# Kernel optimization log

Measured on AMD Instinct MI355X. Metric: run time of the kernel, lower is better.

Reference implementation:

```python
import jax, jax.numpy as jnp
import numpy as np

B_SZ, SEQ_LEN, STATE_DIM, D_IN, D_OUT, KX = 8, 2048, 1024, 512, 512, 10


def setup_inputs() -> dict:
    key = jax.random.key(0)
    ks = jax.random.split(key, 7)
    inputs = jax.random.normal(ks[0], (B_SZ, SEQ_LEN, D_IN), dtype=jnp.float32)
    h0 = jax.random.normal(ks[1], (STATE_DIM,), dtype=jnp.float32)
    # exponential_decay_init(lam=15): x = clamp(-1/lam * log(1-u), max=1); A = (1-x)*sign
    u = jax.random.uniform(ks[2], (STATE_DIM,), dtype=jnp.float32)
    x = jnp.minimum(-(1.0 / 15.0) * jnp.log1p(-u), 1.0)
    sign = jnp.sign(jax.random.normal(ks[3], (STATE_DIM,), dtype=jnp.float32))
    A = (1.0 - x) * sign
    Bm = jax.random.normal(ks[4], (D_IN, STATE_DIM), dtype=jnp.float32) / D_IN
    C = jax.random.normal(ks[5], (STATE_DIM, D_OUT), dtype=jnp.float32) / STATE_DIM
    M = jax.random.normal(ks[6], (D_OUT, D_IN, KX), dtype=jnp.float32) / D_OUT
    return {"inputs": inputs, "h0": h0, "A": A, "B": Bm, "C": C, "M": M}


def _ar_preds(M, x):
    # Equivalent to einsum('oik,bli->bklo') + per-k roll + triu mask + sum over k:
    # ar[b,l,:] = sum_{i=0}^{k-1, i<=l} M[:,:,i] @ x[b, l-i, :]
    b, l, d_in = x.shape
    kx = M.shape[2]
    ar = jnp.einsum('oi,bli->blo', M[:, :, 0], x)
    for i in range(1, kx):
        x_shift = jnp.pad(x, ((0, 0), (i, 0), (0, 0)))[:, :l]  # shift right, zero-fill
        ar = ar + jnp.einsum('oi,bli->blo', M[:, :, i], x_shift)
    return ar


def reference(inputs, h0, A, B, C, M):
    b, l, d_in = inputs.shape
    state_dim = A.shape[0]
    # Project inputs once: u_t @ B for all t -> [b, l, s]
    uB = jnp.einsum('bli,is->bls', inputs, B)

    def step(h, u_t):
        h = A * h + u_t  # diagonal recurrence
        return h, h

    h_init = jnp.broadcast_to(h0, (b, state_dim))
    _, hs = jax.lax.scan(step, h_init, jnp.swapaxes(uB, 0, 1))  # [l, b, s]
    hs = jnp.swapaxes(hs, 0, 1)  # [b, l, s]
    lds_out = hs @ C  # [b, l, d_out]
    return lds_out + _ar_preds(M, inputs)
```

## Files before the change

### kernel.cpp

```cpp
#include <hip/hip_runtime.h>

#define B_SZ   8
#define SEQ    2048
#define PSEQ   (SEQ+16)
#define SDIM   1024
#define DIN    512
#define DOUT   512
#define KX     10
#define RTOT   (B_SZ*SEQ)
#define LC     64
#define NC     (SEQ/LC)

typedef __attribute__((ext_vector_type(8))) short short8;
typedef __attribute__((ext_vector_type(4))) float f32x4;
typedef __attribute__((ext_vector_type(4))) unsigned short bfx4;

#define OFF_XP   0UL
#define OFF_UB   16908288UL
#define OFF_HS   50462720UL
#define OFF_BT   84017152UL
#define OFF_CT   85065728UL
#define OFF_MT   86114304UL

__device__ __forceinline__ short f2bf(float f) {
  unsigned u = __builtin_bit_cast(unsigned, f);
  u += 0x7fffu + ((u >> 16) & 1u);
  return (short)(u >> 16);
}
__device__ __forceinline__ float bf2f(unsigned short b) {
  return __builtin_bit_cast(float, (unsigned)b << 16);
}

#define GLOAD16(gp, lp) __builtin_amdgcn_global_load_lds( \
    (const __attribute__((address_space(1))) void*)(gp), \
    (__attribute__((address_space(3))) void*)(lp), 16, 0, 0)
#define WAITVM(n) asm volatile("s_waitcnt vmcnt(" #n ")" ::: "memory")
#define LGKM0()   do { asm volatile("s_waitcnt lgkmcnt(0)" ::: "memory"); \
                       __builtin_amdgcn_sched_barrier(0); } while (0)
#define SBAR() __builtin_amdgcn_s_barrier()

__global__ void k_conv_x(const float* __restrict__ in, short* __restrict__ out) {
  const int NG = RTOT * (DIN / 8);
  for (int g = blockIdx.x * 256 + threadIdx.x; g < NG; g += 2048 * 256) {
    int r = g >> 6, c8 = g & 63;
    int b = r >> 11, t = r & 2047;
    const float4* p = reinterpret_cast<const float4*>(in) + (size_t)g * 2;
    float4 f0 = p[0], f1 = p[1];
    short8 o;
    o[0]=f2bf(f0.x); o[1]=f2bf(f0.y); o[2]=f2bf(f0.z); o[3]=f2bf(f0.w);
    o[4]=f2bf(f1.x); o[5]=f2bf(f1.y); o[6]=f2bf(f1.z); o[7]=f2bf(f1.w);
    *reinterpret_cast<short8*>(out + ((size_t)(b * PSEQ + 16 + t) * DIN + c8 * 8)) = o;
  }
}

__global__ void k_zero_pad(short* __restrict__ Xp) {
  int idx = blockIdx.x * 256 + threadIdx.x;
  if (idx >= B_SZ * 16 * (DIN / 8)) return;
  int b = idx >> 10, rem = idx & 1023;
  int row16 = rem >> 6, c8 = rem & 63;
  const short8 z = {0,0,0,0,0,0,0,0};
  *reinterpret_cast<short8*>(Xp + ((size_t)(b * PSEQ + row16) * DIN + c8 * 8)) = z;
}

__global__ void k_transpose_bf16(const float* __restrict__ in, short* __restrict__ out,
                                 int rows, int cols) {
  __shared__ float t[32][33];
  int bx = blockIdx.x * 32, by = blockIdx.y * 32;
  int tx = threadIdx.x & 31, ty = threadIdx.x >> 5;
  #pragma unroll
  for (int j = 0; j < 32; j += 8)
    t[ty + j][tx] = in[(size_t)(by + ty + j) * cols + (bx + tx)];
  __syncthreads();
  #pragma unroll
  for (int j = 0; j < 32; j += 8)
    out[(size_t)(bx + ty + j) * rows + (by + tx)] = f2bf(t[tx][ty + j]);
}

__global__ void k_prep_M(const float* __restrict__ M, short* __restrict__ Mt) {
  int idx = blockIdx.x * 256 + threadIdx.x;
  if (idx >= DOUT * DIN) return;
  int o = idx / DIN, i = idx - o * DIN;
  const float* src = M + ((size_t)o * DIN + i) * KX;
  #pragma unroll
  for (int t = 0; t < KX; ++t)
    Mt[((size_t)t * DOUT + o) * DIN + i] = f2bf(src[t]);
}

__global__ void k_scan_E(const short* __restrict__ uB, const float* __restrict__ A,
                         float* __restrict__ E) {
  int blk = blockIdx.x, tid = threadIdx.x;
  int b = blk >> 5, c = blk & 31;
  int s0 = tid * 4;
  const short* base = uB + ((size_t)b * SEQ + (size_t)c * LC) * SDIM + s0;
  float a[4], h[4];
  #pragma unroll
  for (int j = 0; j < 4; ++j) { a[j] = A[s0 + j]; h[j] = 0.f; }
  for (int t = 0; t < LC; ++t) {
    bfx4 v = *reinterpret_cast<const bfx4*>(base + (size_t)t * SDIM);
    #pragma unroll
    for (int j = 0; j < 4; ++j) h[j] = fmaf(a[j], h[j], bf2f(v[j]));
  }
  float* ep = E + (size_t)blk * SDIM + s0;
  #pragma unroll
  for (int j = 0; j < 4; ++j) ep[j] = h[j];
}

__global__ void k_scan_S(const float* __restrict__ E, const float* __restrict__ A,
                         const float* __restrict__ h0, float* __restrict__ Sb) {
  int blk = blockIdx.x, tid = threadIdx.x;
  int b = blk >> 2;
  int s = ((blk & 3) << 8) + tid;
  float a = A[s], ap = a;
  #pragma unroll
  for (int q = 0; q < 6; ++q) ap *= ap;
  float S = h0[s];
  for (int c = 0; c < NC; ++c) {
    size_t idx = ((size_t)b * NC + c) * SDIM + s;
    Sb[idx] = S;
    S = fmaf(ap, S, E[idx]);
  }
}

__global__ void k_scan_h(const short* __restrict__ uB, const float* __restrict__ A,
                         const float* __restrict__ Sb, short* __restrict__ hs) {
  int blk = blockIdx.x, tid = threadIdx.x;
  int b = blk >> 5, c = blk & 31;
  int s0 = tid * 4;
  const short* base = uB + ((size_t)b * SEQ + (size_t)c * LC) * SDIM + s0;
  short* hbase = hs + ((size_t)b * SEQ + (size_t)c * LC) * SDIM + s0;
  float a[4], h[4];
  #pragma unroll
  for (int j = 0; j < 4; ++j) {
    a[j] = A[s0 + j];
    h[j] = Sb[(size_t)blk * SDIM + s0 + j];
  }
  for (int t = 0; t < LC; ++t) {
    bfx4 v = *reinterpret_cast<const bfx4*>(base + (size_t)t * SDIM);
    bfx4 o;
    #pragma unroll
    for (int j = 0; j < 4; ++j) {
      h[j] = fmaf(a[j], h[j], bf2f(v[j]));
      o[j] = (unsigned short)f2bf(h[j]);
    }
    *reinterpret_cast<bfx4*>(hbase + (size_t)t * SDIM) = o;
  }
}

__device__ __forceinline__ void stage128(const short* __restrict__ g, int ld,
                                         short* l, int tid) {
  int rsub = tid >> 3;
  int slot = (tid & 7) ^ (rsub & 7);
  #pragma unroll
  for (int i = 0; i < 4; ++i) {
    int row = i * 32 + rsub;
    GLOAD16(g + (size_t)row * ld + slot * 8, l + row * 64 + (tid & 7) * 8);
  }
}

__device__ __forceinline__ void mfma_tile(const short* lA, int aoff, const short* lB,
                                          int lane, int wm, int wn, f32x4 acc[4][4]) {
  int lr = lane & 15;
  int h  = lane >> 4;
  #pragma unroll
  for (int kk = 0; kk < 2; ++kk) {
    int kslot = kk * 4 + h;
    short8 af[4], bfr[4];
    #pragma unroll
    for (int mi = 0; mi < 4; ++mi) {
      int row = aoff + wm * 64 + mi * 16 + lr;
      af[mi] = *reinterpret_cast<const short8*>(lA + row * 64 + ((kslot ^ (row & 7)) << 3));
    }
    #pragma unroll
    for (int ni = 0; ni < 4; ++ni) {
      int row = wn * 64 + ni * 16 + lr;
      bfr[ni] = *reinterpret_cast<const short8*>(lB + row * 64 + ((kslot ^ (row & 7)) << 3));
    }
    __builtin_amdgcn_s_setprio(1);
    #pragma unroll
    for (int mi = 0; mi < 4; ++mi)
      #pragma unroll
      for (int ni = 0; ni < 4; ++ni)
        acc[mi][ni] = __builtin_amdgcn_mfma_f32_16x16x32_bf16(af[mi], bfr[ni], acc[mi][ni], 0, 0, 0);
    __builtin_amdgcn_s_setprio(0);
  }
}

__global__ __launch_bounds__(256) void k_gemm_uB(const short* __restrict__ Xp,
                                                 const short* __restrict__ Bt,
                                                 short* __restrict__ uB) {
  __shared__ __attribute__((aligned(16))) short lds[32768];
  short* A0 = lds;         short* B0 = lds + 8192;
  short* A1 = lds + 16384; short* B1 = lds + 24576;
  int tid = threadIdx.x, lane = tid & 63, w = tid >> 6, wm = w >> 1, wn = w & 1;
  long r0 = (long)blockIdx.x * 128;
  int  c0 = blockIdx.y * 128;
  int  b  = (int)(r0 >> 11);
  const short* Abase = Xp + (size_t)(r0 + 16 * (b + 1)) * DIN;
  const short* Bbase = Bt + (size_t)c0 * DIN;
  const f32x4 z4 = {0.f, 0.f, 0.f, 0.f};
  f32x4 acc[4][4];
  #pragma unroll
  for (int mi = 0; mi < 4; ++mi)
    #pragma unroll
    for (int ni = 0; ni < 4; ++ni) acc[mi][ni] = z4;

  stage128(Abase, DIN, A0, tid);      stage128(Bbase, DIN, B0, tid);
  stage128(Abase + 64, DIN, A1, tid); stage128(Bbase + 64, DIN, B1, tid);
  WAITVM(8);
  SBAR();
  for (int kt = 0; kt < 8; ++kt) {
    const short* a  = (kt & 1) ? A1 : A0;
    const short* bb = (kt & 1) ? B1 : B0;
    mfma_tile(a, 0, bb, lane, wm, wn, acc);
    SBAR();
    if (kt + 2 < 8) {
      short* ad = (kt & 1) ? A1 : A0;
      short* bd = (kt & 1) ? B1 : B0;
      stage128(Abase + (kt + 2) * 64, DIN, ad, tid);
      stage128(Bbase + (kt + 2) * 64, DIN, bd, tid);
      WAITVM(8);
    } else {
      WAITVM(0);
    }
    SBAR();
  }
  #pragma unroll
  for (int mi = 0; mi < 4; ++mi)
    #pragma unroll
    for (int ni = 0; ni < 4; ++ni)
      #pragma unroll
      for (int r = 0; r < 4; ++r) {
        long row = r0 + wm * 64 + mi * 16 + (lane >> 4) * 4 + r;
        int  col = c0 + wn * 64 + ni * 16 + (lane & 15);
        uB[(size_t)row * SDIM + col] = f2bf(acc[mi][ni][r]);
      }
}


__device__ __forceinline__ void stageA256(const short* __restrict__ g, int ld,
                                          short* l, int tid) {
  int rsub = tid >> 3;
  int slot = (tid & 7) ^ (rsub & 7);
  #pragma unroll
  for (int i = 0; i < 4; ++i) {
    int row = i * 64 + rsub;
    GLOAD16(g + (size_t)row * ld + slot * 8, l + row * 64 + (tid & 7) * 8);
  }
}
__device__ __forceinline__ void stageB128(const short* __restrict__ g, int ld,
                                          short* l, int tid) {
  int rsub = tid >> 3;
  int slot = (tid & 7) ^ (rsub & 7);
  #pragma unroll
  for (int i = 0; i < 2; ++i) {
    int row = i * 64 + rsub;
    GLOAD16(g + (size_t)row * ld + slot * 8, l + row * 64 + (tid & 7) * 8);
  }
}
__device__ __forceinline__ void stageX272(const short* __restrict__ g, int ld,
                                          short* l, int tid) {
  stageA256(g, ld, l, tid);
  if (tid < 128) {
    int rsub = tid >> 3;
    int row = 256 + rsub;
    int slot = (tid & 7) ^ (row & 7);
    GLOAD16(g + (size_t)row * ld + slot * 8, l + row * 64 + (tid & 7) * 8);
  }
}

__device__ __forceinline__ void compute_step(const short* la, int aoff, const short* lb,
                                             int lane, int wm, int wn, f32x4 acc[4][4]) {
  int lr = lane & 15;
  int h  = lane >> 4;
  short8 af[4][2], bfr[4][2];
  #pragma unroll
  for (int kk = 0; kk < 2; ++kk) {
    int kslot = kk * 4 + h;
    #pragma unroll
    for (int mi = 0; mi < 4; ++mi) {
      int row = aoff + wm * 64 + mi * 16 + lr;
      af[mi][kk] = *reinterpret_cast<const short8*>(la + row * 64 + ((kslot ^ (row & 7)) << 3));
    }
    #pragma unroll
    for (int ni = 0; ni < 4; ++ni) {
      int row = wn * 64 + ni * 16 + lr;
      bfr[ni][kk] = *reinterpret_cast<const short8*>(lb + row * 64 + ((kslot ^ (row & 7)) << 3));
    }
  }
  __builtin_amdgcn_s_setprio(1);
  #pragma unroll
  for (int kk = 0; kk < 2; ++kk)
    #pragma unroll
    for (int mi = 0; mi < 4; ++mi)
      #pragma unroll
      for (int ni = 0; ni < 4; ++ni)
        acc[mi][ni] = __builtin_amdgcn_mfma_f32_16x16x32_bf16(af[mi][kk], bfr[ni][kk], acc[mi][ni], 0, 0, 0);
  __builtin_amdgcn_s_setprio(0);
}

__global__ __launch_bounds__(512) void k_gemm_out(const short* __restrict__ hs,
                                                  const short* __restrict__ Xp,
                                                  const short* __restrict__ Ct,
                                                  const short* __restrict__ Mt,
                                                  float* __restrict__ out) {
  __shared__ __attribute__((aligned(16))) short lds[49152];
  short* A0p = lds;          short* B0p = lds + 16384;
  short* A1p = lds + 24576;  short* B1p = lds + 40960;
  short* Xs  = lds;
  short* M0p = lds + 24576;  short* M1p = lds + 40960;
  int tid = threadIdx.x, lane = tid & 63, w = tid >> 6;
  int wm = w >> 1, wn = w & 1;
  int bid = blockIdx.x;
  int sw  = (bid & 7) * 32 + (bid >> 3);
  long r0 = (long)(sw & 63) * 256;
  int  c0 = (sw >> 6) * 128;
  int  b  = (int)(r0 >> 11);
  const short* hsA = hs + (size_t)r0 * SDIM;
  const short* CtB = Ct + (size_t)c0 * SDIM;
  const short* Xa  = Xp + (size_t)(r0 + 16 * (b + 1) - 16) * DIN;
  const short* MtB = Mt + (size_t)c0 * DIN;

  const f32x4 z4 = {0.f, 0.f, 0.f, 0.f};
  f32x4 acc[4][4];
  #pragma unroll
  for (int mi = 0; mi < 4; ++mi)
    #pragma unroll
    for (int ni = 0; ni < 4; ++ni) acc[mi][ni] = z4;

  stageA256(hsA, SDIM, A0p, tid);
  stageB128(CtB, SDIM, B0p, tid);
  WAITVM(0);
  SBAR();
  for (int s = 0; s < 16; ++s) {
    const short* la = (s & 1) ? A1p : A0p;
    const short* lb = (s & 1) ? B1p : B0p;
    short* na = (s & 1) ? A0p : A1p;
    short* nb = (s & 1) ? B0p : B1p;
    if (s + 1 < 16) {
      stageA256(hsA + (s + 1) * 64, SDIM, na, tid);
      stageB128(CtB + (s + 1) * 64, SDIM, nb, tid);
    } else {
      stageX272(Xa, DIN, Xs, tid);
    }
    compute_step(la, 0, lb, lane, wm, wn, acc);
    LGKM0();
    WAITVM(0);
    SBAR();
  }

  stageB128(MtB, DIN, M0p, tid);
  WAITVM(0);
  SBAR();
  for (int k0 = 0; k0 < 8; ++k0) {
    int kc = k0 * 64;
    for (int tap = 0; tap < KX; ++tap) {
      const short* lm = (tap & 1) ? M1p : M0p;
      short* nm = (tap & 1) ? M0p : M1p;
      if (tap + 1 < KX)
        stageB128(MtB + (size_t)(tap + 1) * DOUT * DIN + kc, DIN, nm, tid);
      else if (k0 + 1 < 8)
        stageB128(MtB + kc + 64, DIN, M0p, tid);
      compute_step(Xs, 16 - tap, lm, lane, wm, wn, acc);
      LGKM0();
      WAITVM(0);
      SBAR();
    }
    if (k0 + 1 < 8) {
      stageX272(Xa + kc + 64, DIN, Xs, tid);
      WAITVM(0);
      SBAR();
    }
  }

  #pragma unroll
  for (int mi = 0; mi < 4; ++mi)
    #pragma unroll
    for (int ni = 0; ni < 4; ++ni)
      #pragma unroll
      for (int r = 0; r < 4; ++r) {
        long row = r0 + wm * 64 + mi * 16 + (lane >> 4) * 4 + r;
        int  col = c0 + wn * 64 + ni * 16 + (lane & 15);
        out[(size_t)row * DOUT + col] = acc[mi][ni][r];
      }
}

extern "C" void kernel_launch(void* const* d_in, const int* in_sizes, int n_in,
                              void* d_out, int out_size, void* d_ws, size_t ws_size,
                              hipStream_t stream) {
  (void)in_sizes; (void)n_in; (void)out_size; (void)ws_size;
  const float* x  = (const float*)d_in[0];
  const float* h0 = (const float*)d_in[1];
  const float* A  = (const float*)d_in[2];
  const float* B  = (const float*)d_in[3];
  const float* C  = (const float*)d_in[4];
  const float* M  = (const float*)d_in[5];
  float* out = (float*)d_out;
  char* ws = (char*)d_ws;

  short* Xp  = (short*)(ws + OFF_XP);
  short* uB  = (short*)(ws + OFF_UB);
  short* hsb = (short*)(ws + OFF_HS);
  short* Bt  = (short*)(ws + OFF_BT);
  short* Ct  = (short*)(ws + OFF_CT);
  short* Mt  = (short*)(ws + OFF_MT);
  float* E   = out;
  float* Sb  = out + B_SZ * NC * SDIM;

  k_conv_x<<<2048, 256, 0, stream>>>(x, Xp);
  k_zero_pad<<<32, 256, 0, stream>>>(Xp);
  k_transpose_bf16<<<dim3(SDIM / 32, DIN / 32), 256, 0, stream>>>(B, Bt, DIN, SDIM);
  k_transpose_bf16<<<dim3(DOUT / 32, SDIM / 32), 256, 0, stream>>>(C, Ct, SDIM, DOUT);
  k_prep_M<<<(DOUT * DIN + 255) / 256, 256, 0, stream>>>(M, Mt);

  k_gemm_uB<<<dim3(RTOT / 128, SDIM / 128), 256, 0, stream>>>(Xp, Bt, uB);

  k_scan_E<<<B_SZ * NC, 256, 0, stream>>>(uB, A, E);
  k_scan_S<<<B_SZ * 4, 256, 0, stream>>>(E, A, h0, Sb);
  k_scan_h<<<B_SZ * NC, 256, 0, stream>>>(uB, A, Sb, hsb);

  k_gemm_out<<<256, 512, 0, stream>>>(hsb, Xp, Ct, Mt, out);
}
```

Measured before the change: 156.4 us.

## Widen output GEMM tile to 256x256 and split K across blocks with atomics

```diff
diff --git a/kernel.cpp b/kernel.cpp
--- a/kernel.cpp
+++ b/kernel.cpp
@@ -35,8 +35,6 @@
     (const __attribute__((address_space(1))) void*)(gp), \
     (__attribute__((address_space(3))) void*)(lp), 16, 0, 0)
 #define WAITVM(n) asm volatile("s_waitcnt vmcnt(" #n ")" ::: "memory")
-#define LGKM0()   do { asm volatile("s_waitcnt lgkmcnt(0)" ::: "memory"); \
-                       __builtin_amdgcn_sched_barrier(0); } while (0)
 #define SBAR() __builtin_amdgcn_s_barrier()
 
 __global__ void k_conv_x(const float* __restrict__ in, short* __restrict__ out) {
@@ -237,8 +235,8 @@
 }
 
 
-__device__ __forceinline__ void stageA256(const short* __restrict__ g, int ld,
-                                          short* l, int tid) {
+__device__ __forceinline__ void stage256(const short* __restrict__ g, int ld,
+                                         short* l, int tid) {
   int rsub = tid >> 3;
   int slot = (tid & 7) ^ (rsub & 7);
   #pragma unroll
@@ -247,19 +245,9 @@
     GLOAD16(g + (size_t)row * ld + slot * 8, l + row * 64 + (tid & 7) * 8);
   }
 }
-__device__ __forceinline__ void stageB128(const short* __restrict__ g, int ld,
-                                          short* l, int tid) {
-  int rsub = tid >> 3;
-  int slot = (tid & 7) ^ (rsub & 7);
-  #pragma unroll
-  for (int i = 0; i < 2; ++i) {
-    int row = i * 64 + rsub;
-    GLOAD16(g + (size_t)row * ld + slot * 8, l + row * 64 + (tid & 7) * 8);
-  }
-}
 __device__ __forceinline__ void stageX272(const short* __restrict__ g, int ld,
                                           short* l, int tid) {
-  stageA256(g, ld, l, tid);
+  stage256(g, ld, l, tid);
   if (tid < 128) {
     int rsub = tid >> 3;
     int row = 256 + rsub;
@@ -268,34 +256,32 @@
   }
 }
 
-__device__ __forceinline__ void compute_step(const short* la, int aoff, const short* lb,
-                                             int lane, int wm, int wn, f32x4 acc[4][4]) {
+__device__ __forceinline__ void compute_step2(const short* la, int aoff, const short* lb,
+                                              int lane, int wm, int wn, f32x4 acc[8][4]) {
   int lr = lane & 15;
   int h  = lane >> 4;
-  short8 af[4][2], bfr[4][2];
   #pragma unroll
   for (int kk = 0; kk < 2; ++kk) {
     int kslot = kk * 4 + h;
-    #pragma unroll
-    for (int mi = 0; mi < 4; ++mi) {
-      int row = aoff + wm * 64 + mi * 16 + lr;
-      af[mi][kk] = *reinterpret_cast<const short8*>(la + row * 64 + ((kslot ^ (row & 7)) << 3));
-    }
+    short8 af[8], bfr[4];
     #pragma unroll
     for (int ni = 0; ni < 4; ++ni) {
       int row = wn * 64 + ni * 16 + lr;
-      bfr[ni][kk] = *reinterpret_cast<const short8*>(lb + row * 64 + ((kslot ^ (row & 7)) << 3));
-    }
-  }
-  __builtin_amdgcn_s_setprio(1);
-  #pragma unroll
-  for (int kk = 0; kk < 2; ++kk)
-    #pragma unroll
-    for (int mi = 0; mi < 4; ++mi)
+      bfr[ni] = *reinterpret_cast<const short8*>(lb + row * 64 + ((kslot ^ (row & 7)) << 3));
+    }
+    #pragma unroll
+    for (int mi = 0; mi < 8; ++mi) {
+      int row = aoff + wm * 128 + mi * 16 + lr;
+      af[mi] = *reinterpret_cast<const short8*>(la + row * 64 + ((kslot ^ (row & 7)) << 3));
+    }
+    __builtin_amdgcn_s_setprio(1);
+    #pragma unroll
+    for (int mi = 0; mi < 8; ++mi)
       #pragma unroll
       for (int ni = 0; ni < 4; ++ni)
-        acc[mi][ni] = __builtin_amdgcn_mfma_f32_16x16x32_bf16(af[mi][kk], bfr[ni][kk], acc[mi][ni], 0, 0, 0);
-  __builtin_amdgcn_s_setprio(0);
+        acc[mi][ni] = __builtin_amdgcn_mfma_f32_16x16x32_bf16(af[mi], bfr[ni], acc[mi][ni], 0, 0, 0);
+    __builtin_amdgcn_s_setprio(0);
+  }
 }
 
 __global__ __launch_bounds__(512) void k_gemm_out(const short* __restrict__ hs,
@@ -303,17 +289,19 @@
                                                   const short* __restrict__ Ct,
                                                   const short* __restrict__ Mt,
                                                   float* __restrict__ out) {
-  __shared__ __attribute__((aligned(16))) short lds[49152];
+  __shared__ __attribute__((aligned(16))) short lds[65536];
   short* A0p = lds;          short* B0p = lds + 16384;
-  short* A1p = lds + 24576;  short* B1p = lds + 40960;
+  short* A1p = lds + 32768;  short* B1p = lds + 49152;
   short* Xs  = lds;
-  short* M0p = lds + 24576;  short* M1p = lds + 40960;
+  short* M0p = lds + 32768;  short* M1p = lds + 49152;
   int tid = threadIdx.x, lane = tid & 63, w = tid >> 6;
-  int wm = w >> 1, wn = w & 1;
+  int wm = w & 1, wn = w >> 1;
   int bid = blockIdx.x;
   int sw  = (bid & 7) * 32 + (bid >> 3);
-  long r0 = (long)(sw & 63) * 256;
-  int  c0 = (sw >> 6) * 128;
+  int rowblk = sw & 63, combo = sw >> 6;
+  long r0 = (long)rowblk * 256;
+  int  c0 = (combo & 1) * 256;
+  int  khalf = combo >> 1;
   int  b  = (int)(r0 >> 11);
   const short* hsA = hs + (size_t)r0 * SDIM;
   const short* CtB = Ct + (size_t)c0 * SDIM;
@@ -321,47 +309,56 @@
   const short* MtB = Mt + (size_t)c0 * DIN;
 
   const f32x4 z4 = {0.f, 0.f, 0.f, 0.f};
-  f32x4 acc[4][4];
-  #pragma unroll
-  for (int mi = 0; mi < 4; ++mi)
+  f32x4 acc[8][4];
+  #pragma unroll
+  for (int mi = 0; mi < 8; ++mi)
     #pragma unroll
     for (int ni = 0; ni < 4; ++ni) acc[mi][ni] = z4;
 
-  stageA256(hsA, SDIM, A0p, tid);
-  stageB128(CtB, SDIM, B0p, tid);
-  WAITVM(0);
-  SBAR();
-  for (int s = 0; s < 16; ++s) {
-    const short* la = (s & 1) ? A1p : A0p;
-    const short* lb = (s & 1) ? B1p : B0p;
-    short* na = (s & 1) ? A0p : A1p;
-    short* nb = (s & 1) ? B0p : B1p;
-    if (s + 1 < 16) {
-      stageA256(hsA + (s + 1) * 64, SDIM, na, tid);
-      stageB128(CtB + (s + 1) * 64, SDIM, nb, tid);
-    } else {
-      stageX272(Xa, DIN, Xs, tid);
-    }
-    compute_step(la, 0, lb, lane, wm, wn, acc);
-    LGKM0();
+  int tap_lo, tap_hi;
+  if (khalf == 0) {
+    tap_lo = 0; tap_hi = 3;
+    stage256(hsA, SDIM, A0p, tid);
+    stage256(CtB, SDIM, B0p, tid);
     WAITVM(0);
     SBAR();
-  }
-
-  stageB128(MtB, DIN, M0p, tid);
-  WAITVM(0);
-  SBAR();
+    for (int s = 0; s < 16; ++s) {
+      const short* la = (s & 1) ? A1p : A0p;
+      const short* lb = (s & 1) ? B1p : B0p;
+      short* na = (s & 1) ? A0p : A1p;
+      short* nb = (s & 1) ? B0p : B1p;
+      if (s + 1 < 16) {
+        stage256(hsA + (s + 1) * 64, SDIM, na, tid);
+        stage256(CtB + (s + 1) * 64, SDIM, nb, tid);
+      } else {
+        stageX272(Xa, DIN, Xs, tid);
+      }
+      compute_step2(la, 0, lb, lane, wm, wn, acc);
+      WAITVM(0);
+      SBAR();
+    }
+    stage256(MtB, DIN, M0p, tid);
+    WAITVM(0);
+    SBAR();
+  } else {
+    tap_lo = 4; tap_hi = 9;
+    stageX272(Xa, DIN, Xs, tid);
+    stage256(MtB + (size_t)4 * DOUT * DIN, DIN, M0p, tid);
+    WAITVM(0);
+    SBAR();
+  }
+
   for (int k0 = 0; k0 < 8; ++k0) {
     int kc = k0 * 64;
-    for (int tap = 0; tap < KX; ++tap) {
-      const short* lm = (tap & 1) ? M1p : M0p;
-      short* nm = (tap & 1) ? M0p : M1p;
-      if (tap + 1 < KX)
-        stageB128(MtB + (size_t)(tap + 1) * DOUT * DIN + kc, DIN, nm, tid);
+    for (int j = 0; j <= tap_hi - tap_lo; ++j) {
+      int tap = tap_lo + j;
+      const short* lm = (j & 1) ? M1p : M0p;
+      short* nm = (j & 1) ? M0p : M1p;
+      if (tap < tap_hi)
+        stage256(MtB + (size_t)(tap + 1) * DOUT * DIN + kc, DIN, nm, tid);
       else if (k0 + 1 < 8)
-        stageB128(MtB + kc + 64, DIN, M0p, tid);
-      compute_step(Xs, 16 - tap, lm, lane, wm, wn, acc);
-      LGKM0();
+        stage256(MtB + (size_t)tap_lo * DOUT * DIN + kc + 64, DIN, nm, tid);
+      compute_step2(Xs, 16 - tap, lm, lane, wm, wn, acc);
       WAITVM(0);
       SBAR();
     }
@@ -373,14 +370,14 @@
   }
 
   #pragma unroll
-  for (int mi = 0; mi < 4; ++mi)
+  for (int mi = 0; mi < 8; ++mi)
     #pragma unroll
     for (int ni = 0; ni < 4; ++ni)
       #pragma unroll
       for (int r = 0; r < 4; ++r) {
-        long row = r0 + wm * 64 + mi * 16 + (lane >> 4) * 4 + r;
+        long row = r0 + wm * 128 + mi * 16 + (lane >> 4) * 4 + r;
         int  col = c0 + wn * 64 + ni * 16 + (lane & 15);
-        out[(size_t)row * DOUT + col] = acc[mi][ni][r];
+        atomicAdd(&out[(size_t)row * DOUT + col], acc[mi][ni][r]);
       }
 }
 
@@ -418,5 +415,7 @@
   k_scan_S<<<B_SZ * 4, 256, 0, stream>>>(E, A, h0, Sb);
   k_scan_h<<<B_SZ * NC, 256, 0, stream>>>(uB, A, Sb, hsb);
 
+  hipMemsetAsync(out, 0, (size_t)RTOT * DOUT * sizeof(float), stream);
+
   k_gemm_out<<<256, 512, 0, stream>>>(hsb, Xp, Ct, Mt, out);
 }
```

After: 201.4 us. 28.8% more time.

## Deepen k_gemm_out pipeline to two-ahead prefetch with partial vmcnt waits

Applied to the files above, without the earlier changes.

```diff
diff --git a/kernel.cpp b/kernel.cpp
--- a/kernel.cpp
+++ b/kernel.cpp
@@ -35,8 +35,6 @@
     (const __attribute__((address_space(1))) void*)(gp), \
     (__attribute__((address_space(3))) void*)(lp), 16, 0, 0)
 #define WAITVM(n) asm volatile("s_waitcnt vmcnt(" #n ")" ::: "memory")
-#define LGKM0()   do { asm volatile("s_waitcnt lgkmcnt(0)" ::: "memory"); \
-                       __builtin_amdgcn_sched_barrier(0); } while (0)
 #define SBAR() __builtin_amdgcn_s_barrier()
 
 __global__ void k_conv_x(const float* __restrict__ in, short* __restrict__ out) {
@@ -303,11 +301,11 @@
                                                   const short* __restrict__ Ct,
                                                   const short* __restrict__ Mt,
                                                   float* __restrict__ out) {
-  __shared__ __attribute__((aligned(16))) short lds[49152];
+  __shared__ __attribute__((aligned(16))) short lds[51200];
   short* A0p = lds;          short* B0p = lds + 16384;
   short* A1p = lds + 24576;  short* B1p = lds + 40960;
-  short* Xs  = lds;
-  short* M0p = lds + 24576;  short* M1p = lds + 40960;
+  short* Xs0 = lds;          short* Xs1 = lds + 17408;
+  short* M0p = lds + 34816;  short* M1p = lds + 43008;
   int tid = threadIdx.x, lane = tid & 63, w = tid >> 6;
   int wm = w >> 1, wn = w & 1;
   int bid = blockIdx.x;
@@ -329,45 +327,55 @@
 
   stageA256(hsA, SDIM, A0p, tid);
   stageB128(CtB, SDIM, B0p, tid);
-  WAITVM(0);
+  stageA256(hsA + 64, SDIM, A1p, tid);
+  stageB128(CtB + 64, SDIM, B1p, tid);
+  WAITVM(6);
   SBAR();
   for (int s = 0; s < 16; ++s) {
     const short* la = (s & 1) ? A1p : A0p;
     const short* lb = (s & 1) ? B1p : B0p;
-    short* na = (s & 1) ? A0p : A1p;
-    short* nb = (s & 1) ? B0p : B1p;
-    if (s + 1 < 16) {
-      stageA256(hsA + (s + 1) * 64, SDIM, na, tid);
-      stageB128(CtB + (s + 1) * 64, SDIM, nb, tid);
+    compute_step(la, 0, lb, lane, wm, wn, acc);
+    SBAR();
+    if (s + 2 < 16) {
+      short* na = (s & 1) ? A1p : A0p;
+      short* nb = (s & 1) ? B1p : B0p;
+      stageA256(hsA + (s + 2) * 64, SDIM, na, tid);
+      stageB128(CtB + (s + 2) * 64, SDIM, nb, tid);
+      WAITVM(6);
+    } else if (s == 14) {
+      stageX272(Xa, DIN, Xs0, tid);
+      WAITVM(4);
     } else {
-      stageX272(Xa, DIN, Xs, tid);
-    }
-    compute_step(la, 0, lb, lane, wm, wn, acc);
-    LGKM0();
-    WAITVM(0);
+      stageB128(MtB, DIN, M0p, tid);
+      stageB128(MtB + (size_t)DOUT * DIN, DIN, M1p, tid);
+      WAITVM(2);
+    }
     SBAR();
   }
 
-  stageB128(MtB, DIN, M0p, tid);
-  WAITVM(0);
-  SBAR();
   for (int k0 = 0; k0 < 8; ++k0) {
+    const short* xs = (k0 & 1) ? Xs1 : Xs0;
+    short*       xn = (k0 & 1) ? Xs0 : Xs1;
     int kc = k0 * 64;
-    for (int tap = 0; tap < KX; ++tap) {
-      const short* lm = (tap & 1) ? M1p : M0p;
-      short* nm = (tap & 1) ? M0p : M1p;
-      if (tap + 1 < KX)
-        stageB128(MtB + (size_t)(tap + 1) * DOUT * DIN + kc, DIN, nm, tid);
-      else if (k0 + 1 < 8)
-        stageB128(MtB + kc + 64, DIN, M0p, tid);
-      compute_step(Xs, 16 - tap, lm, lane, wm, wn, acc);
-      LGKM0();
-      WAITVM(0);
+    bool lastslice = (k0 == 7);
+    for (int j = 0; j < KX; ++j) {
+      const short* lm = (j & 1) ? M1p : M0p;
+      short*       nm = (j & 1) ? M1p : M0p;
+      compute_step(xs, 16 - j, lm, lane, wm, wn, acc);
       SBAR();
-    }
-    if (k0 + 1 < 8) {
-      stageX272(Xa + kc + 64, DIN, Xs, tid);
-      WAITVM(0);
+      if (j + 2 < KX)
+        stageB128(MtB + (size_t)(j + 2) * DOUT * DIN + kc, DIN, nm, tid);
+      else if (!lastslice)
+        stageB128(MtB + (size_t)(j + 2 - KX) * DOUT * DIN + kc + 64, DIN, nm, tid);
+      if (j == 1 && !lastslice)
+        stageX272(Xa + kc + 64, DIN, xn, tid);
+      if ((j == 1 || j == 2) && !lastslice) {
+        WAITVM(6);
+      } else if (j + 2 < KX || !lastslice) {
+        WAITVM(2);
+      } else {
+        WAITVM(0);
+      }
       SBAR();
     }
   }
```

Result: no change. 156.0 us (-0.3%).
